# Optimization experiments

Hardware: AMD Instinct MI355X
Metric: run time of the kernel (lower is better)

## Reference

```python
import jax, jax.numpy as jnp
import numpy as np

B, N_VEC, N_DIM, N_W, N_HID, VOCAB, N_CLASS = 16, 2048, 32, 4, 128, 32000, 10


def setup_inputs() -> dict:
    key = jax.random.key(0)
    ks = jax.random.split(key, 8)
    data = jax.random.randint(ks[0], (B, N_VEC), 0, VOCAB, dtype=jnp.int64)
    emb = jax.random.normal(ks[1], (VOCAB, N_DIM), dtype=jnp.float32) * 0.1
    # stacked per-layer weights for the n_W WModules: Linear(n_dim->n_hid), GELU, Linear(n_hid->n_vec)
    fw1 = jax.random.normal(ks[2], (N_W, N_DIM, N_HID), dtype=jnp.float32) * (1.0 / np.sqrt(N_DIM))
    fb1 = jnp.zeros((N_W, N_HID), dtype=jnp.float32)
    fw2 = jax.random.normal(ks[3], (N_W, N_HID, N_VEC), dtype=jnp.float32) * (1.0 / np.sqrt(N_HID))
    fb2 = jnp.zeros((N_W, N_VEC), dtype=jnp.float32)
    Wf = jax.random.normal(ks[4], (N_VEC * N_DIM, N_CLASS), dtype=jnp.float32) * (1.0 / np.sqrt(N_VEC * N_DIM))
    bf = jnp.zeros((N_CLASS,), dtype=jnp.float32)
    return {"data": data, "emb": emb, "fw1": fw1, "fb1": fb1, "fw2": fw2, "fb2": fb2, "Wf": Wf, "bf": bf}


def reference(data, emb, fw1, fb1, fw2, fb2, Wf, bf):
    X = emb[data]                       # [B, n_vec, n_dim]
    V = X                               # g is identity (with_g=False)
    # iterate over self.fs[::-1]: indices n_W-1 .. 0
    for i in range(N_W - 1, -1, -1):
        h = jax.nn.gelu(jnp.einsum('bnd,dh->bnh', X, fw1[i]) + fb1[i], approximate=False)
        W = jnp.einsum('bnh,hm->bnm', h, fw2[i]) + fb2[i]   # [B, n_vec, n_vec]
        V = jnp.einsum('bnm,bmd->bnd', W, V)                # [B, n_vec, n_dim]
    out = V.reshape(V.shape[0], -1) @ Wf + bf               # [B, n_class]
    return out
```

## Files before the change

kernel.cpp:

```cpp
#include <hip/hip_runtime.h>

#define NB 16
#define NVEC 2048
#define NDIM 32
#define NW 4
#define NHID 128
#define NCLASS 10
#define MS 16
#define USIZE (129 * 32)

__device__ __forceinline__ float gelu_fast(float x) {
    float t = 1.5957691216057308f * x * (1.0f + 0.044715f * x * x);
    return x / (1.0f + __expf(-t));
}

__global__ __launch_bounds__(256) void k_embed(const int* __restrict__ data,
                                               const float* __restrict__ emb,
                                               const float* __restrict__ bf,
                                               float* __restrict__ X,
                                               float* __restrict__ out) {
    int gid = blockIdx.x * 256 + threadIdx.x;
    int row = gid >> 3, sub = gid & 7;
    ((float4*)X)[gid] = ((const float4*)emb)[data[row] * 8 + sub];
    if (blockIdx.x == 0 && threadIdx.x < NB * NCLASS)
        out[threadIdx.x] = bf[threadIdx.x % NCLASS];
}

__global__ __launch_bounds__(1024) void k_U(const float* __restrict__ V,
                                            const float* __restrict__ fw2,
                                            const float* __restrict__ fb2,
                                            float* __restrict__ Upart) {
    __shared__ float Vs[128 * 32];
    __shared__ float cred[4][33];
    int ms = blockIdx.x, b = blockIdx.y;
    int tid = threadIdx.x;
    int m0 = ms * 128;
    ((float4*)Vs)[tid] = ((const float4*)(V + (b * NVEC + m0) * NDIM))[tid];
    int k1 = tid & 127, d0 = (tid >> 7) * 4;
    const float* wrow = fw2 + k1 * NVEC + m0;
    float acc[4] = {0.f, 0.f, 0.f, 0.f};
    __syncthreads();
#pragma unroll
    for (int mt = 0; mt < 128; mt += 16) {
        float4 w4[4];
#pragma unroll
        for (int j = 0; j < 4; ++j) w4[j] = ((const float4*)(wrow + mt))[j];
        const float* wf = (const float*)w4;
#pragma unroll
        for (int j = 0; j < 16; ++j) {
            float w = wf[j];
            float4 v = *(const float4*)&Vs[(mt + j) * 32 + d0];
            acc[0] += w * v.x; acc[1] += w * v.y;
            acc[2] += w * v.z; acc[3] += w * v.w;
        }
    }
    float* Up = Upart + ((size_t)ms * NB + b) * USIZE;
    *(float4*)&Up[k1 * 32 + d0] = make_float4(acc[0], acc[1], acc[2], acc[3]);
    if (tid < 128) {
        int d = tid & 31, seg = tid >> 5;
        float ca = 0.f;
#pragma unroll 8
        for (int mm = seg * 32; mm < seg * 32 + 32; ++mm)
            ca += fb2[m0 + mm] * Vs[mm * 32 + d];
        cred[seg][d] = ca;
    }
    __syncthreads();
    if (tid < 32)
        Up[128 * 32 + tid] = cred[0][tid] + cred[1][tid] + cred[2][tid] + cred[3][tid];
}

__global__ __launch_bounds__(256) void k_Ured(const float* __restrict__ Upart,
                                              float* __restrict__ U) {
    int b = blockIdx.x;
    int i4 = blockIdx.y * 129 + threadIdx.x;
    if (threadIdx.x >= 129) return;
    float4 s = ((const float4*)Upart)[(size_t)b * (USIZE / 4) + i4];
#pragma unroll
    for (int ms = 1; ms < MS; ++ms) {
        float4 v = ((const float4*)Upart)[((size_t)ms * NB + b) * (USIZE / 4) + i4];
        s.x += v.x; s.y += v.y; s.z += v.z; s.w += v.w;
    }
    ((float4*)U)[b * (USIZE / 4) + i4] = s;
}

template <bool LAST>
__global__ __launch_bounds__(256) void k_applyF(const float* __restrict__ X,
                                                const float* __restrict__ fw1l,
                                                const float* __restrict__ fb1l,
                                                const float* __restrict__ U,
                                                float* __restrict__ Vout,
                                                const float* __restrict__ Wf,
                                                float* __restrict__ out) {
    __shared__ float Us[USIZE];
    __shared__ float w1s[NDIM * NHID];
    __shared__ float xs[64][33];
    __shared__ float hs[64 * 132];
    __shared__ float ored[4][NCLASS];
    int ng = blockIdx.x, b = blockIdx.y;
    int tid = threadIdx.x;
    int n0 = ng * 64;

    for (int i4 = tid; i4 < USIZE / 4; i4 += 256)
        ((float4*)Us)[i4] = ((const float4*)(U + (size_t)b * USIZE))[i4];
#pragma unroll
    for (int j = 0; j < 4; ++j)
        ((float4*)w1s)[tid + j * 256] = ((const float4*)fw1l)[tid + j * 256];
#pragma unroll
    for (int j = 0; j < 2; ++j) {
        int i4 = tid + j * 256;
        float4 v = ((const float4*)(X + (b * NVEC + n0) * NDIM))[i4];
        int r = i4 >> 3, c4 = (i4 & 7) * 4;
        xs[r][c4] = v.x; xs[r][c4 + 1] = v.y;
        xs[r][c4 + 2] = v.z; xs[r][c4 + 3] = v.w;
    }
    __syncthreads();

    {
        int kg = tid & 15, rg = tid >> 4;
        int k0 = kg * 8, r0 = rg * 4;
        float acc[4][8];
#pragma unroll
        for (int j = 0; j < 8; ++j) {
            float bv = fb1l[k0 + j];
            acc[0][j] = bv; acc[1][j] = bv; acc[2][j] = bv; acc[3][j] = bv;
        }
#pragma unroll 8
        for (int d = 0; d < NDIM; ++d) {
            float4 wa = *(const float4*)&w1s[d * NHID + k0];
            float4 wb = *(const float4*)&w1s[d * NHID + k0 + 4];
            float wk[8] = {wa.x, wa.y, wa.z, wa.w, wb.x, wb.y, wb.z, wb.w};
            float x0 = xs[r0][d], x1 = xs[r0 + 1][d];
            float x2 = xs[r0 + 2][d], x3 = xs[r0 + 3][d];
#pragma unroll
            for (int j = 0; j < 8; ++j) {
                acc[0][j] += x0 * wk[j];
                acc[1][j] += x1 * wk[j];
                acc[2][j] += x2 * wk[j];
                acc[3][j] += x3 * wk[j];
            }
        }
#pragma unroll
        for (int r = 0; r < 4; ++r) {
            float4 o0, o1;
            o0.x = gelu_fast(acc[r][0]); o0.y = gelu_fast(acc[r][1]);
            o0.z = gelu_fast(acc[r][2]); o0.w = gelu_fast(acc[r][3]);
            o1.x = gelu_fast(acc[r][4]); o1.y = gelu_fast(acc[r][5]);
            o1.z = gelu_fast(acc[r][6]); o1.w = gelu_fast(acc[r][7]);
            *(float4*)&hs[(r0 + r) * 132 + k0] = o0;
            *(float4*)&hs[(r0 + r) * 132 + k0 + 4] = o1;
        }
    }
    __syncthreads();

    {
        int dg = tid & 7, rga = tid >> 3;
        int d0 = dg * 4, r0 = rga * 2;
        float4 a0 = *(const float4*)&Us[NHID * 32 + d0];
        float4 a1 = a0;
#pragma unroll 8
        for (int k = 0; k < NHID; k += 4) {
            float4 h0 = *(const float4*)&hs[r0 * 132 + k];
            float4 h1 = *(const float4*)&hs[(r0 + 1) * 132 + k];
            float4 u0 = *(const float4*)&Us[(k + 0) * 32 + d0];
            float4 u1 = *(const float4*)&Us[(k + 1) * 32 + d0];
            float4 u2 = *(const float4*)&Us[(k + 2) * 32 + d0];
            float4 u3 = *(const float4*)&Us[(k + 3) * 32 + d0];
            a0.x += h0.x * u0.x + h0.y * u1.x + h0.z * u2.x + h0.w * u3.x;
            a0.y += h0.x * u0.y + h0.y * u1.y + h0.z * u2.y + h0.w * u3.y;
            a0.z += h0.x * u0.z + h0.y * u1.z + h0.z * u2.z + h0.w * u3.z;
            a0.w += h0.x * u0.w + h0.y * u1.w + h0.z * u2.w + h0.w * u3.w;
            a1.x += h1.x * u0.x + h1.y * u1.x + h1.z * u2.x + h1.w * u3.x;
            a1.y += h1.x * u0.y + h1.y * u1.y + h1.z * u2.y + h1.w * u3.y;
            a1.z += h1.x * u0.z + h1.y * u1.z + h1.z * u2.z + h1.w * u3.z;
            a1.w += h1.x * u0.w + h1.y * u1.w + h1.z * u2.w + h1.w * u3.w;
        }
        if constexpr (!LAST) {
            *(float4*)&Vout[(b * NVEC + n0 + r0) * NDIM + d0] = a0;
            *(float4*)&Vout[(b * NVEC + n0 + r0 + 1) * NDIM + d0] = a1;
        } else {
            float accC[NCLASS];
#pragma unroll
            for (int c = 0; c < NCLASS; ++c) accC[c] = 0.f;
            float va[2][4] = {{a0.x, a0.y, a0.z, a0.w}, {a1.x, a1.y, a1.z, a1.w}};
#pragma unroll
            for (int r = 0; r < 2; ++r)
#pragma unroll
                for (int dd = 0; dd < 4; ++dd) {
                    int jj = (n0 + r0 + r) * NDIM + d0 + dd;
                    const float2* wr = (const float2*)(Wf + (size_t)jj * NCLASS);
                    float v = va[r][dd];
#pragma unroll
                    for (int p = 0; p < 5; ++p) {
                        float2 w = wr[p];
                        accC[2 * p]     += v * w.x;
                        accC[2 * p + 1] += v * w.y;
                    }
                }
            int lane = tid & 63, wv = tid >> 6;
#pragma unroll
            for (int c = 0; c < NCLASS; ++c)
#pragma unroll
                for (int off = 32; off >= 1; off >>= 1)
                    accC[c] += __shfl_down(accC[c], off, 64);
            if (lane == 0) {
#pragma unroll
                for (int c = 0; c < NCLASS; ++c) ored[wv][c] = accC[c];
            }
            __syncthreads();
            if (tid < NCLASS)
                atomicAdd(&out[b * NCLASS + tid],
                          ored[0][tid] + ored[1][tid] + ored[2][tid] + ored[3][tid]);
        }
    }
}

extern "C" void kernel_launch(void* const* d_in, const int* in_sizes, int n_in,
                              void* d_out, int out_size, void* d_ws, size_t ws_size,
                              hipStream_t stream) {
    const int*   data = (const int*)d_in[0];
    const float* emb  = (const float*)d_in[1];
    const float* fw1  = (const float*)d_in[2];
    const float* fb1  = (const float*)d_in[3];
    const float* fw2  = (const float*)d_in[4];
    const float* fb2  = (const float*)d_in[5];
    const float* Wf   = (const float*)d_in[6];
    const float* bf   = (const float*)d_in[7];
    float* out = (float*)d_out;

    float* X     = (float*)d_ws;
    float* VA    = X + NB * NVEC * NDIM;
    float* VB    = VA + NB * NVEC * NDIM;
    float* Upart = VB + NB * NVEC * NDIM;
    float* U     = Upart + (size_t)MS * NB * USIZE;

    k_embed<<<dim3(NB * NVEC * NDIM / 4 / 256), 256, 0, stream>>>(data, emb, bf, X, out);

    const float* Vcur = X;
    float* Vnext = VA;
    for (int t = 0; t < NW; ++t) {
        int i = NW - 1 - t;
        k_U<<<dim3(MS, NB), 1024, 0, stream>>>(Vcur, fw2 + (size_t)i * NHID * NVEC,
                                               fb2 + (size_t)i * NVEC, Upart);
        k_Ured<<<dim3(NB, 8), 256, 0, stream>>>(Upart, U);
        if (i > 0) {
            k_applyF<false><<<dim3(NVEC / 64, NB), 256, 0, stream>>>(
                X, fw1 + (size_t)i * NDIM * NHID, fb1 + (size_t)i * NHID,
                U, Vnext, nullptr, nullptr);
            Vcur = Vnext;
            Vnext = (Vnext == VA) ? VB : VA;
        } else {
            k_applyF<true><<<dim3(NVEC / 64, NB), 256, 0, stream>>>(
                X, fw1, fb1, U, nullptr, Wf, out);
        }
    }
}
```

Measured before the change: 219.6 us.

## Precompute GELU hidden activations for all layers upfront and stream them in apply

The embedding gather is fused with computing h = GELU(X·fw1+fb1) for all four layers in one launch, writing them to a global buffer. The per-layer apply kernel then only reads h and U, with no shared-memory staging. The U kernel is retiled to 256 threads over 64-row slices with register blocking, which doubles the partial count (MS=32), and the reduce grid is adjusted to match. This removes the repeated per-layer first GEMM from the serial chain, at the cost of writing and re-reading a 4×16×2048×128 float buffer (about 64 MB) through global memory.

```diff
diff --git a/kernel.cpp b/kernel.cpp
--- a/kernel.cpp
+++ b/kernel.cpp
@@ -6,211 +6,227 @@
 #define NW 4
 #define NHID 128
 #define NCLASS 10
-#define MS 16
+#define MS 32
 #define USIZE (129 * 32)
+#define HSLICE ((size_t)NB * NVEC * NHID)
 
 __device__ __forceinline__ float gelu_fast(float x) {
     float t = 1.5957691216057308f * x * (1.0f + 0.044715f * x * x);
     return x / (1.0f + __expf(-t));
 }
 
-__global__ __launch_bounds__(256) void k_embed(const int* __restrict__ data,
-                                               const float* __restrict__ emb,
-                                               const float* __restrict__ bf,
-                                               float* __restrict__ X,
-                                               float* __restrict__ out) {
-    int gid = blockIdx.x * 256 + threadIdx.x;
-    int row = gid >> 3, sub = gid & 7;
-    ((float4*)X)[gid] = ((const float4*)emb)[data[row] * 8 + sub];
-    if (blockIdx.x == 0 && threadIdx.x < NB * NCLASS)
-        out[threadIdx.x] = bf[threadIdx.x % NCLASS];
-}
-
-__global__ __launch_bounds__(1024) void k_U(const float* __restrict__ V,
-                                            const float* __restrict__ fw2,
-                                            const float* __restrict__ fb2,
-                                            float* __restrict__ Upart) {
-    __shared__ float Vs[128 * 32];
-    __shared__ float cred[4][33];
+__global__ __launch_bounds__(256) void k_hx(const int* __restrict__ data,
+                                            const float* __restrict__ emb,
+                                            const float* __restrict__ fw1,
+                                            const float* __restrict__ fb1,
+                                            const float* __restrict__ bf,
+                                            float* __restrict__ hbuf,
+                                            float* __restrict__ X,
+                                            float* __restrict__ out) {
+    int chunk = blockIdx.x, b = blockIdx.y, l = blockIdx.z;
+    int tid = threadIdx.x;
+    int n0 = chunk * 64;
+    const float* w1 = fw1 + (size_t)l * NDIM * NHID;
+    const float* b1 = fb1 + (size_t)l * NHID;
+
+    int kgrp = tid & 15, rgrp = tid >> 4;
+    int k0 = kgrp * 8, r0 = rgrp * 4;
+    int idx[4];
+#pragma unroll
+    for (int rr = 0; rr < 4; ++rr) idx[rr] = data[b * NVEC + n0 + r0 + rr];
+
+    float acc[4][8];
+    {
+        float4 bv0 = *(const float4*)&b1[k0];
+        float4 bv1 = *(const float4*)&b1[k0 + 4];
+        float bk[8] = {bv0.x, bv0.y, bv0.z, bv0.w, bv1.x, bv1.y, bv1.z, bv1.w};
+#pragma unroll
+        for (int rr = 0; rr < 4; ++rr)
+#pragma unroll
+            for (int j = 0; j < 8; ++j) acc[rr][j] = bk[j];
+    }
+#pragma unroll 2
+    for (int d = 0; d < NDIM; d += 4) {
+        float4 xr[4];
+#pragma unroll
+        for (int rr = 0; rr < 4; ++rr)
+            xr[rr] = *(const float4*)&emb[(size_t)idx[rr] * NDIM + d];
+#pragma unroll
+        for (int dd = 0; dd < 4; ++dd) {
+            float4 wa = *(const float4*)&w1[(d + dd) * NHID + k0];
+            float4 wb = *(const float4*)&w1[(d + dd) * NHID + k0 + 4];
+            float wk[8] = {wa.x, wa.y, wa.z, wa.w, wb.x, wb.y, wb.z, wb.w};
+#pragma unroll
+            for (int rr = 0; rr < 4; ++rr) {
+                float xv = ((const float*)&xr[rr])[dd];
+#pragma unroll
+                for (int j = 0; j < 8; ++j) acc[rr][j] += xv * wk[j];
+            }
+        }
+    }
+    float* hp = hbuf + (size_t)l * HSLICE + ((size_t)b * NVEC + n0 + r0) * NHID + k0;
+#pragma unroll
+    for (int rr = 0; rr < 4; ++rr) {
+        float4 o0, o1;
+        o0.x = gelu_fast(acc[rr][0]); o0.y = gelu_fast(acc[rr][1]);
+        o0.z = gelu_fast(acc[rr][2]); o0.w = gelu_fast(acc[rr][3]);
+        o1.x = gelu_fast(acc[rr][4]); o1.y = gelu_fast(acc[rr][5]);
+        o1.z = gelu_fast(acc[rr][6]); o1.w = gelu_fast(acc[rr][7]);
+        *(float4*)(hp + rr * NHID)     = o0;
+        *(float4*)(hp + rr * NHID + 4) = o1;
+    }
+    if (l == 0) {
+        float4* Xo = (float4*)(X + ((size_t)b * NVEC + n0) * NDIM);
+#pragma unroll
+        for (int j = 0; j < 2; ++j) {
+            int i4 = tid + j * 256;
+            int r = i4 >> 3, c = i4 & 7;
+            Xo[i4] = ((const float4*)emb)[(size_t)data[b * NVEC + n0 + r] * 8 + c];
+        }
+        if (chunk == 0 && b == 0 && tid < NB * NCLASS)
+            out[tid] = bf[tid % NCLASS];
+    }
+}
+
+__global__ __launch_bounds__(256) void k_U(const float* __restrict__ V,
+                                           const float* __restrict__ fw2,
+                                           const float* __restrict__ fb2,
+                                           float* __restrict__ Upart) {
     int ms = blockIdx.x, b = blockIdx.y;
-    int tid = threadIdx.x;
-    int m0 = ms * 128;
-    ((float4*)Vs)[tid] = ((const float4*)(V + (b * NVEC + m0) * NDIM))[tid];
-    int k1 = tid & 127, d0 = (tid >> 7) * 4;
-    const float* wrow = fw2 + k1 * NVEC + m0;
-    float acc[4] = {0.f, 0.f, 0.f, 0.f};
-    __syncthreads();
-#pragma unroll
-    for (int mt = 0; mt < 128; mt += 16) {
-        float4 w4[4];
-#pragma unroll
-        for (int j = 0; j < 4; ++j) w4[j] = ((const float4*)(wrow + mt))[j];
-        const float* wf = (const float*)w4;
-#pragma unroll
-        for (int j = 0; j < 16; ++j) {
-            float w = wf[j];
-            float4 v = *(const float4*)&Vs[(mt + j) * 32 + d0];
-            acc[0] += w * v.x; acc[1] += w * v.y;
-            acc[2] += w * v.z; acc[3] += w * v.w;
+    int tid = threadIdx.x, lane = tid & 63, w = tid >> 6;
+    int m0 = ms * 64;
+    int kgrp = lane & 7, dgrp = lane >> 3;
+    int k0 = w * 32 + kgrp * 4, d0 = dgrp * 4;
+    const float* Vb = V + ((size_t)b * NVEC + m0) * NDIM;
+
+    float acc[4][4];
+#pragma unroll
+    for (int kk = 0; kk < 4; ++kk)
+#pragma unroll
+        for (int j = 0; j < 4; ++j) acc[kk][j] = 0.f;
+
+#pragma unroll 4
+    for (int mm = 0; mm < 64; mm += 4) {
+        float4 wr[4], vr[4];
+#pragma unroll
+        for (int kk = 0; kk < 4; ++kk)
+            wr[kk] = *(const float4*)&fw2[(size_t)(k0 + kk) * NVEC + m0 + mm];
+#pragma unroll
+        for (int j = 0; j < 4; ++j)
+            vr[j] = *(const float4*)&Vb[(mm + j) * NDIM + d0];
+#pragma unroll
+        for (int kk = 0; kk < 4; ++kk) {
+            const float* wf = (const float*)&wr[kk];
+#pragma unroll
+            for (int j = 0; j < 4; ++j) {
+                float wv = wf[j];
+                acc[kk][0] += wv * vr[j].x;
+                acc[kk][1] += wv * vr[j].y;
+                acc[kk][2] += wv * vr[j].z;
+                acc[kk][3] += wv * vr[j].w;
+            }
         }
     }
     float* Up = Upart + ((size_t)ms * NB + b) * USIZE;
-    *(float4*)&Up[k1 * 32 + d0] = make_float4(acc[0], acc[1], acc[2], acc[3]);
-    if (tid < 128) {
-        int d = tid & 31, seg = tid >> 5;
+#pragma unroll
+    for (int kk = 0; kk < 4; ++kk)
+        *(float4*)&Up[(k0 + kk) * 32 + d0] =
+            make_float4(acc[kk][0], acc[kk][1], acc[kk][2], acc[kk][3]);
+    if (tid < 32) {
         float ca = 0.f;
 #pragma unroll 8
-        for (int mm = seg * 32; mm < seg * 32 + 32; ++mm)
-            ca += fb2[m0 + mm] * Vs[mm * 32 + d];
-        cred[seg][d] = ca;
-    }
-    __syncthreads();
-    if (tid < 32)
-        Up[128 * 32 + tid] = cred[0][tid] + cred[1][tid] + cred[2][tid] + cred[3][tid];
+        for (int mm = 0; mm < 64; ++mm)
+            ca += fb2[m0 + mm] * Vb[mm * NDIM + tid];
+        Up[128 * 32 + tid] = ca;
+    }
 }
 
 __global__ __launch_bounds__(256) void k_Ured(const float* __restrict__ Upart,
                                               float* __restrict__ U) {
     int b = blockIdx.x;
-    int i4 = blockIdx.y * 129 + threadIdx.x;
-    if (threadIdx.x >= 129) return;
-    float4 s = ((const float4*)Upart)[(size_t)b * (USIZE / 4) + i4];
+    int i4 = blockIdx.y * 256 + threadIdx.x;
+    if (i4 >= USIZE / 4) return;
+    float4 s = ((const float4*)(Upart + (size_t)b * USIZE))[i4];
 #pragma unroll
     for (int ms = 1; ms < MS; ++ms) {
-        float4 v = ((const float4*)Upart)[((size_t)ms * NB + b) * (USIZE / 4) + i4];
+        float4 v = ((const float4*)(Upart + ((size_t)ms * NB + b) * USIZE))[i4];
         s.x += v.x; s.y += v.y; s.z += v.z; s.w += v.w;
     }
-    ((float4*)U)[b * (USIZE / 4) + i4] = s;
+    ((float4*)(U + (size_t)b * USIZE))[i4] = s;
 }
 
 template <bool LAST>
-__global__ __launch_bounds__(256) void k_applyF(const float* __restrict__ X,
-                                                const float* __restrict__ fw1l,
-                                                const float* __restrict__ fb1l,
-                                                const float* __restrict__ U,
-                                                float* __restrict__ Vout,
-                                                const float* __restrict__ Wf,
-                                                float* __restrict__ out) {
-    __shared__ float Us[USIZE];
-    __shared__ float w1s[NDIM * NHID];
-    __shared__ float xs[64][33];
-    __shared__ float hs[64 * 132];
+__global__ __launch_bounds__(256) void k_apply(const float* __restrict__ hl,
+                                               const float* __restrict__ U,
+                                               float* __restrict__ Vout,
+                                               const float* __restrict__ Wf,
+                                               float* __restrict__ out) {
     __shared__ float ored[4][NCLASS];
     int ng = blockIdx.x, b = blockIdx.y;
-    int tid = threadIdx.x;
+    int tid = threadIdx.x, lane = tid & 63, w = tid >> 6;
     int n0 = ng * 64;
-
-    for (int i4 = tid; i4 < USIZE / 4; i4 += 256)
-        ((float4*)Us)[i4] = ((const float4*)(U + (size_t)b * USIZE))[i4];
-#pragma unroll
-    for (int j = 0; j < 4; ++j)
-        ((float4*)w1s)[tid + j * 256] = ((const float4*)fw1l)[tid + j * 256];
-#pragma unroll
-    for (int j = 0; j < 2; ++j) {
-        int i4 = tid + j * 256;
-        float4 v = ((const float4*)(X + (b * NVEC + n0) * NDIM))[i4];
-        int r = i4 >> 3, c4 = (i4 & 7) * 4;
-        xs[r][c4] = v.x; xs[r][c4 + 1] = v.y;
-        xs[r][c4 + 2] = v.z; xs[r][c4 + 3] = v.w;
-    }
-    __syncthreads();
-
-    {
-        int kg = tid & 15, rg = tid >> 4;
-        int k0 = kg * 8, r0 = rg * 4;
-        float acc[4][8];
-#pragma unroll
-        for (int j = 0; j < 8; ++j) {
-            float bv = fb1l[k0 + j];
-            acc[0][j] = bv; acc[1][j] = bv; acc[2][j] = bv; acc[3][j] = bv;
-        }
-#pragma unroll 8
-        for (int d = 0; d < NDIM; ++d) {
-            float4 wa = *(const float4*)&w1s[d * NHID + k0];
-            float4 wb = *(const float4*)&w1s[d * NHID + k0 + 4];
-            float wk[8] = {wa.x, wa.y, wa.z, wa.w, wb.x, wb.y, wb.z, wb.w};
-            float x0 = xs[r0][d], x1 = xs[r0 + 1][d];
-            float x2 = xs[r0 + 2][d], x3 = xs[r0 + 3][d];
-#pragma unroll
-            for (int j = 0; j < 8; ++j) {
-                acc[0][j] += x0 * wk[j];
-                acc[1][j] += x1 * wk[j];
-                acc[2][j] += x2 * wk[j];
-                acc[3][j] += x3 * wk[j];
+    int dgrp = lane & 7, rgrp = lane >> 3;
+    int d0 = dgrp * 4;
+    int row = n0 + w * 16 + rgrp * 2;
+    const float* Ub = U + (size_t)b * USIZE;
+    const float* h0 = hl + ((size_t)b * NVEC + row) * NHID;
+    const float* h1 = h0 + NHID;
+
+    float4 a0 = *(const float4*)&Ub[128 * 32 + d0];
+    float4 a1 = a0;
+#pragma unroll 4
+    for (int k = 0; k < NHID; k += 4) {
+        float4 hq0 = *(const float4*)&h0[k];
+        float4 hq1 = *(const float4*)&h1[k];
+        float4 u0 = *(const float4*)&Ub[(k + 0) * 32 + d0];
+        float4 u1 = *(const float4*)&Ub[(k + 1) * 32 + d0];
+        float4 u2 = *(const float4*)&Ub[(k + 2) * 32 + d0];
+        float4 u3 = *(const float4*)&Ub[(k + 3) * 32 + d0];
+        a0.x += hq0.x * u0.x + hq0.y * u1.x + hq0.z * u2.x + hq0.w * u3.x;
+        a0.y += hq0.x * u0.y + hq0.y * u1.y + hq0.z * u2.y + hq0.w * u3.y;
+        a0.z += hq0.x * u0.z + hq0.y * u1.z + hq0.z * u2.z + hq0.w * u3.z;
+        a0.w += hq0.x * u0.w + hq0.y * u1.w + hq0.z * u2.w + hq0.w * u3.w;
+        a1.x += hq1.x * u0.x + hq1.y * u1.x + hq1.z * u2.x + hq1.w * u3.x;
+        a1.y += hq1.x * u0.y + hq1.y * u1.y + hq1.z * u2.y + hq1.w * u3.y;
+        a1.z += hq1.x * u0.z + hq1.y * u1.z + hq1.z * u2.z + hq1.w * u3.z;
+        a1.w += hq1.x * u0.w + hq1.y * u1.w + hq1.z * u2.w + hq1.w * u3.w;
+    }
+    if constexpr (!LAST) {
+        float* vo = Vout + ((size_t)b * NVEC + row) * NDIM + d0;
+        *(float4*)vo          = a0;
+        *(float4*)(vo + NDIM) = a1;
+    } else {
+        float accC[NCLASS];
+#pragma unroll
+        for (int c = 0; c < NCLASS; ++c) accC[c] = 0.f;
+        float va[2][4] = {{a0.x, a0.y, a0.z, a0.w}, {a1.x, a1.y, a1.z, a1.w}};
+#pragma unroll
+        for (int r = 0; r < 2; ++r)
+#pragma unroll
+            for (int dd = 0; dd < 4; ++dd) {
+                size_t j = (size_t)(row + r) * NDIM + d0 + dd;
+                const float2* wr = (const float2*)(Wf + j * NCLASS);
+                float v = va[r][dd];
+#pragma unroll
+                for (int p = 0; p < 5; ++p) {
+                    float2 wv = wr[p];
+                    accC[2 * p]     += v * wv.x;
+                    accC[2 * p + 1] += v * wv.y;
+                }
             }
-        }
-#pragma unroll
-        for (int r = 0; r < 4; ++r) {
-            float4 o0, o1;
-            o0.x = gelu_fast(acc[r][0]); o0.y = gelu_fast(acc[r][1]);
-            o0.z = gelu_fast(acc[r][2]); o0.w = gelu_fast(acc[r][3]);
-            o1.x = gelu_fast(acc[r][4]); o1.y = gelu_fast(acc[r][5]);
-            o1.z = gelu_fast(acc[r][6]); o1.w = gelu_fast(acc[r][7]);
-            *(float4*)&hs[(r0 + r) * 132 + k0] = o0;
-            *(float4*)&hs[(r0 + r) * 132 + k0 + 4] = o1;
-        }
-    }
-    __syncthreads();
-
-    {
-        int dg = tid & 7, rga = tid >> 3;
-        int d0 = dg * 4, r0 = rga * 2;
-        float4 a0 = *(const float4*)&Us[NHID * 32 + d0];
-        float4 a1 = a0;
-#pragma unroll 8
-        for (int k = 0; k < NHID; k += 4) {
-            float4 h0 = *(const float4*)&hs[r0 * 132 + k];
-            float4 h1 = *(const float4*)&hs[(r0 + 1) * 132 + k];
-            float4 u0 = *(const float4*)&Us[(k + 0) * 32 + d0];
-            float4 u1 = *(const float4*)&Us[(k + 1) * 32 + d0];
-            float4 u2 = *(const float4*)&Us[(k + 2) * 32 + d0];
-            float4 u3 = *(const float4*)&Us[(k + 3) * 32 + d0];
-            a0.x += h0.x * u0.x + h0.y * u1.x + h0.z * u2.x + h0.w * u3.x;
-            a0.y += h0.x * u0.y + h0.y * u1.y + h0.z * u2.y + h0.w * u3.y;
-            a0.z += h0.x * u0.z + h0.y * u1.z + h0.z * u2.z + h0.w * u3.z;
-            a0.w += h0.x * u0.w + h0.y * u1.w + h0.z * u2.w + h0.w * u3.w;
-            a1.x += h1.x * u0.x + h1.y * u1.x + h1.z * u2.x + h1.w * u3.x;
-            a1.y += h1.x * u0.y + h1.y * u1.y + h1.z * u2.y + h1.w * u3.y;
-            a1.z += h1.x * u0.z + h1.y * u1.z + h1.z * u2.z + h1.w * u3.z;
-            a1.w += h1.x * u0.w + h1.y * u1.w + h1.z * u2.w + h1.w * u3.w;
-        }
-        if constexpr (!LAST) {
-            *(float4*)&Vout[(b * NVEC + n0 + r0) * NDIM + d0] = a0;
-            *(float4*)&Vout[(b * NVEC + n0 + r0 + 1) * NDIM + d0] = a1;
-        } else {
-            float accC[NCLASS];
-#pragma unroll
-            for (int c = 0; c < NCLASS; ++c) accC[c] = 0.f;
-            float va[2][4] = {{a0.x, a0.y, a0.z, a0.w}, {a1.x, a1.y, a1.z, a1.w}};
-#pragma unroll
-            for (int r = 0; r < 2; ++r)
-#pragma unroll
-                for (int dd = 0; dd < 4; ++dd) {
-                    int jj = (n0 + r0 + r) * NDIM + d0 + dd;
-                    const float2* wr = (const float2*)(Wf + (size_t)jj * NCLASS);
-                    float v = va[r][dd];
-#pragma unroll
-                    for (int p = 0; p < 5; ++p) {
-                        float2 w = wr[p];
-                        accC[2 * p]     += v * w.x;
-                        accC[2 * p + 1] += v * w.y;
-                    }
-                }
-            int lane = tid & 63, wv = tid >> 6;
-#pragma unroll
-            for (int c = 0; c < NCLASS; ++c)
-#pragma unroll
-                for (int off = 32; off >= 1; off >>= 1)
-                    accC[c] += __shfl_down(accC[c], off, 64);
-            if (lane == 0) {
-#pragma unroll
-                for (int c = 0; c < NCLASS; ++c) ored[wv][c] = accC[c];
-            }
-            __syncthreads();
-            if (tid < NCLASS)
-                atomicAdd(&out[b * NCLASS + tid],
-                          ored[0][tid] + ored[1][tid] + ored[2][tid] + ored[3][tid]);
-        }
+#pragma unroll
+        for (int c = 0; c < NCLASS; ++c)
+#pragma unroll
+            for (int off = 32; off >= 1; off >>= 1)
+                accC[c] += __shfl_down(accC[c], off, 64);
+        if (lane == 0) {
+#pragma unroll
+            for (int c = 0; c < NCLASS; ++c) ored[w][c] = accC[c];
+        }
+        __syncthreads();
+        if (tid < NCLASS)
+            atomicAdd(&out[b * NCLASS + tid],
+                      ored[0][tid] + ored[1][tid] + ored[2][tid] + ored[3][tid]);
     }
 }
 
@@ -228,29 +244,31 @@
     float* out = (float*)d_out;
 
     float* X     = (float*)d_ws;
-    float* VA    = X + NB * NVEC * NDIM;
-    float* VB    = VA + NB * NVEC * NDIM;
-    float* Upart = VB + NB * NVEC * NDIM;
+    float* VA    = X + (size_t)NB * NVEC * NDIM;
+    float* VB    = VA + (size_t)NB * NVEC * NDIM;
+    float* Upart = VB + (size_t)NB * NVEC * NDIM;
     float* U     = Upart + (size_t)MS * NB * USIZE;
-
-    k_embed<<<dim3(NB * NVEC * NDIM / 4 / 256), 256, 0, stream>>>(data, emb, bf, X, out);
+    float* hbuf  = U + (size_t)NB * USIZE;
+
+    k_hx<<<dim3(NVEC / 64, NB, NW), 256, 0, stream>>>(data, emb, fw1, fb1, bf,
+                                                      hbuf, X, out);
 
     const float* Vcur = X;
     float* Vnext = VA;
     for (int t = 0; t < NW; ++t) {
         int i = NW - 1 - t;
-        k_U<<<dim3(MS, NB), 1024, 0, stream>>>(Vcur, fw2 + (size_t)i * NHID * NVEC,
-                                               fb2 + (size_t)i * NVEC, Upart);
-        k_Ured<<<dim3(NB, 8), 256, 0, stream>>>(Upart, U);
+        k_U<<<dim3(MS, NB), 256, 0, stream>>>(Vcur, fw2 + (size_t)i * NHID * NVEC,
+                                              fb2 + (size_t)i * NVEC, Upart);
+        k_Ured<<<dim3(NB, 5), 256, 0, stream>>>(Upart, U);
+        const float* hl = hbuf + (size_t)i * HSLICE;
         if (i > 0) {
-            k_applyF<false><<<dim3(NVEC / 64, NB), 256, 0, stream>>>(
-                X, fw1 + (size_t)i * NDIM * NHID, fb1 + (size_t)i * NHID,
-                U, Vnext, nullptr, nullptr);
+            k_apply<false><<<dim3(NVEC / 64, NB), 256, 0, stream>>>(
+                hl, U, Vnext, nullptr, nullptr);
             Vcur = Vnext;
             Vnext = (Vnext == VA) ? VB : VA;
         } else {
-            k_applyF<true><<<dim3(NVEC / 64, NB), 256, 0, stream>>>(
-                X, fw1, fb1, U, nullptr, Wf, out);
-        }
-    }
-}
+            k_apply<true><<<dim3(NVEC / 64, NB), 256, 0, stream>>>(
+                hl, U, nullptr, Wf, out);
+        }
+    }
+}
```

Measured after the change: 305.0 us. 1.39x slower.
